# Kernel tuning notes

Measured on AMD Instinct MI355X. Metric: run time of the kernel, lower is better.

The kernel has to match this reference:

```python
import jax, jax.numpy as jnp
import numpy as np

DIM = 192
HEADS = 6
WS = (6, 12)          # (lat, lon) window
INPUT_SHAPE = (186, 360)
TOW = INPUT_SHAPE[0] // WS[0]   # 31 latitude window types
N_WIN = WS[0] * WS[1]           # 72 tokens per window


def _position_index():
    """Earth-specific relative-position index (static, numpy)."""
    ws0, ws1 = WS
    coords_hi = np.arange(ws0)
    coords_hj = -np.arange(ws0) * ws0
    coords_w = np.arange(ws1)
    c1 = np.stack(np.meshgrid(coords_hi, coords_w, indexing='ij'))  # (2, ws0, ws1)
    c2 = np.stack(np.meshgrid(coords_hj, coords_w, indexing='ij'))
    f1 = c1.reshape(2, -1)
    f2 = c2.reshape(2, -1)
    coords = f1[:, :, None] - f2[:, None, :]      # (2, N, N)
    coords = coords.transpose(1, 2, 0).copy()     # (N, N, 2)
    coords[:, :, 1] += ws1 - 1                    # shift lon diff to >= 0
    coords[:, :, 0] *= 2 * ws1 - 1                # row stride in bias table
    return jnp.asarray(coords.sum(-1).reshape(-1))  # (N*N,) int


def setup_inputs() -> dict:
    key = jax.random.key(0)
    ks = jax.random.split(key, 6)
    B = 2
    nW = INPUT_SHAPE[1] // WS[1]          # 30
    B_ = B * TOW * nW                     # 1860
    table_rows = (2 * WS[1] - 1) * WS[0] * WS[0]  # 828
    return {
        "x": jax.random.normal(ks[0], (B_, N_WIN, DIM), dtype=jnp.float32),
        "mask": jnp.zeros((nW, N_WIN, N_WIN), dtype=jnp.float32),
        "w_qkv": jax.random.normal(ks[1], (DIM, 3 * DIM), dtype=jnp.float32) * 0.02,
        "b_qkv": jnp.zeros((3 * DIM,), dtype=jnp.float32),
        "w_out": jax.random.normal(ks[2], (DIM, DIM), dtype=jnp.float32) * 0.02,
        "b_out": jnp.zeros((DIM,), dtype=jnp.float32),
        "bias_table": jax.random.normal(ks[3], (table_rows, TOW, HEADS), dtype=jnp.float32) * 0.02,
    }


def reference(x, mask, w_qkv, b_qkv, w_out, b_out, bias_table):
    B_, N, dim = x.shape
    hd = dim // HEADS
    scale = hd ** -0.5
    # fused QKV projection
    qkv = (x @ w_qkv + b_qkv).reshape(B_, N, 3, HEADS, hd)
    qkv = qkv.transpose(2, 0, 3, 1, 4)            # (3, B_, H, N, hd)
    q, k, v = qkv[0] * scale, qkv[1], qkv[2]
    attn = jnp.einsum('bhnd,bhmd->bhnm', q, k)    # (B_, H, N, N)
    # earth-specific bias: gather table rows by relative-position index,
    # tiled across the window batch exactly as the torch code's .repeat()
    rep = B_ // TOW
    pos = _position_index()                       # (N*N,)
    bias = bias_table[jnp.tile(pos, rep)]         # (rep*N*N, TOW, H)
    bias = bias.reshape(N, N, -1, HEADS).transpose(2, 3, 0, 1)  # (B_, H, N, N)
    attn = attn + bias
    # window mask (broadcast over groups of nW lon-windows)
    nW = mask.shape[0]
    attn = attn.reshape(B_ // nW, nW, HEADS, N, N) + mask[None, :, None]
    attn = attn.reshape(B_, HEADS, N, N)
    attn = jax.nn.softmax(attn, axis=-1)          # dropout is identity (p=0 / eval)
    out = jnp.einsum('bhnm,bhmd->bhnd', attn, v)  # (B_, H, N, hd)
    out = out.transpose(0, 2, 1, 3).reshape(B_, N, dim)
    return out @ w_out + b_out
```

## Files before the change

kernel.cpp:

```cpp
#include <hip/hip_runtime.h>
#include <cstddef>

typedef short bf16x8 __attribute__((ext_vector_type(8)));
typedef float f32x4  __attribute__((ext_vector_type(4)));

namespace {
constexpr float QSCALE = 0.17677669529663687f;

constexpr size_t BQKV_OFF = 0;
constexpr size_t WOUT_OFF = 576 * 384 * 2;
constexpr size_t BQG_OFF  = WOUT_OFF + 192 * 384 * 2;

constexpr int AXS   = 392;
constexpr int AX_H  = 0;
constexpr int Q2A_H = 72 * AXS;
constexpr int K2A_H = Q2A_H + 6 * 72 * 32;
constexpr int V2A_H = K2A_H + 6 * 72 * 40;
constexpr int HALF_TOT = V2A_H + 6 * 32 * 104;
constexpr int PB_H  = 828 * 6 * 2;
constexpr int LDSA_BYTES = HALF_TOT * 2;
}

__device__ __forceinline__ unsigned short f2bf(float f) {
  unsigned int u = __builtin_bit_cast(unsigned int, f);
  return (unsigned short)((u + 0x7FFFu + ((u >> 16) & 1u)) >> 16);
}
__device__ __forceinline__ float bf2f(unsigned short h) {
  unsigned int u = ((unsigned int)h) << 16;
  return __builtin_bit_cast(float, u);
}
__device__ __forceinline__ int moffv(int i) { return (i < 4) ? i * 16 : 56; }

__global__ __launch_bounds__(256)
void prep_kernel(const float* __restrict__ wqkv, const float* __restrict__ bqkv,
                 const float* __restrict__ wout, unsigned char* __restrict__ ws) {
  int t = blockIdx.x * 256 + threadIdx.x;
  unsigned short* Bq = (unsigned short*)(ws + BQKV_OFF);
  unsigned short* Bo = (unsigned short*)(ws + WOUT_OFF);
  float* bqg = (float*)(ws + BQG_OFF);
  if (t < 576 * 384) {
    int n = t / 384, kk = t % 384;
    int ksrc = kk % 192, part = kk / 192;
    int h = n / 96, r96 = n % 96, kind = r96 / 32, d = r96 % 32;
    float w = wqkv[(size_t)ksrc * 576 + kind * 192 + h * 32 + d];
    if (kind == 0) w *= QSCALE;
    unsigned short hi = f2bf(w);
    Bq[t] = part ? f2bf(w - bf2f(hi)) : hi;
  } else if (t < 576 * 384 + 192 * 384) {
    int t2 = t - 576 * 384;
    int n = t2 / 384, kk = t2 % 384, ksrc = kk % 192, part = kk / 192;
    float w = wout[(size_t)ksrc * 192 + n];
    unsigned short hi = f2bf(w);
    Bo[t2] = part ? f2bf(w - bf2f(hi)) : hi;
  } else if (t < 576 * 384 + 192 * 384 + 576) {
    int n = t - (576 * 384 + 192 * 384);
    int h = n / 96, r96 = n % 96, kind = r96 / 32, d = r96 % 32;
    float b = bqkv[kind * 192 + h * 32 + d];
    if (kind == 0) b *= QSCALE;
    bqg[n] = b;
  }
}

template<int NM>
__device__ __forceinline__ void qkv_wave(unsigned short* sm, const unsigned short* __restrict__ Bq,
                                         const float* __restrict__ bqg, int ntb3, int m0idx,
                                         int lanen, int quad) {
  #pragma unroll 1
  for (int p = 0; p < 3; ++p) {
    const int nbase = 192 * p;
    f32x4 acc[3][NM];
    #pragma unroll
    for (int nt = 0; nt < 3; ++nt)
      #pragma unroll
      for (int mi = 0; mi < NM; ++mi)
        acc[nt][mi] = (f32x4){0.f, 0.f, 0.f, 0.f};
    #pragma unroll 1
    for (int reg = 0; reg < 3; ++reg) {
      const int ab = (reg == 2) ? 192 : 0;
      const int bb = (reg == 1) ? 192 : 0;
      bf16x8 a[NM][6];
      #pragma unroll
      for (int mi = 0; mi < NM; ++mi) {
        const unsigned short* ap = sm + AX_H + (moffv(m0idx + mi) + lanen) * AXS + ab + quad * 8;
        #pragma unroll
        for (int s = 0; s < 6; ++s)
          a[mi][s] = *(const bf16x8*)(ap + 32 * s);
      }
      #pragma unroll
      for (int nt = 0; nt < 3; ++nt) {
        const unsigned short* bp = Bq + (size_t)(nbase + (ntb3 + nt) * 16 + lanen) * 384 + bb + quad * 8;
        #pragma unroll
        for (int s = 0; s < 6; ++s) {
          bf16x8 bfr = *(const bf16x8*)(bp + 32 * s);
          #pragma unroll
          for (int mi = 0; mi < NM; ++mi)
            acc[nt][mi] = __builtin_amdgcn_mfma_f32_16x16x32_bf16(a[mi][s], bfr, acc[nt][mi], 0, 0, 0);
        }
      }
    }
    #pragma unroll 1
    for (int nt = 0; nt < 3; ++nt) {
      const int ng = ntb3 + nt;
      const float bias = bqg[nbase + ng * 16 + lanen];
      const int hh = 2 * p + (ng >= 6 ? 1 : 0);
      const int w96 = (ng % 6) * 16;
      #pragma unroll
      for (int mi = 0; mi < NM; ++mi) {
        const int mo = moffv(m0idx + mi);
        if (w96 < 64) {
          unsigned short* dst;
          int stride, d;
          if (w96 < 32) { dst = sm + Q2A_H + hh * 2304; stride = 32; d = w96 + lanen; }
          else          { dst = sm + K2A_H + hh * 2880; stride = 40; d = w96 - 32 + lanen; }
          #pragma unroll
          for (int r = 0; r < 4; ++r)
            dst[(mo + quad * 4 + r) * stride + d] = f2bf(acc[nt][mi][r] + bias);
        } else {
          const int d = w96 - 64 + lanen;
          ushort4 hv;
          hv.x = f2bf(acc[nt][mi][0] + bias); hv.y = f2bf(acc[nt][mi][1] + bias);
          hv.z = f2bf(acc[nt][mi][2] + bias); hv.w = f2bf(acc[nt][mi][3] + bias);
          *(ushort4*)(sm + V2A_H + hh * 3328 + d * 104 + mo + quad * 4) = hv;
        }
      }
    }
  }
}

__global__ __launch_bounds__(512)
__attribute__((amdgpu_waves_per_eu(2, 2)))
void attn_kernel(const float* __restrict__ x, const float* __restrict__ mask,
                 const float* __restrict__ btab, const unsigned char* __restrict__ ws,
                 float* __restrict__ out) {
  extern __shared__ unsigned short sm[];
  const int w = blockIdx.x, tid = threadIdx.x;
  const int lane = tid & 63, ty = tid >> 6;
  const int lanen = lane & 15, quad = lane >> 4;
  const int mrow = w % 30, tlat = w % 31, w31 = w / 31;
  const float* xw = x + (size_t)w * (72 * 192);
  const float* maskw = mask + (size_t)mrow * (72 * 72);
  const unsigned short* Bq = (const unsigned short*)(ws + BQKV_OFF);
  const float* bqg = (const float*)(ws + BQG_OFF);

  for (int i = tid; i < 3456; i += 512) {
    int r = i / 48, c4 = i % 48;
    float4 v = *(const float4*)(xw + r * 192 + c4 * 4);
    unsigned short h0 = f2bf(v.x), h1 = f2bf(v.y), h2 = f2bf(v.z), h3 = f2bf(v.w);
    ushort4 hv; hv.x = h0; hv.y = h1; hv.z = h2; hv.w = h3;
    ushort4 lv;
    lv.x = f2bf(v.x - bf2f(h0)); lv.y = f2bf(v.y - bf2f(h1));
    lv.z = f2bf(v.z - bf2f(h2)); lv.w = f2bf(v.w - bf2f(h3));
    *(ushort4*)(sm + AX_H + r * AXS + c4 * 4) = hv;
    *(ushort4*)(sm + AX_H + r * AXS + 192 + c4 * 4) = lv;
  }
  for (int i = tid; i < 9984; i += 512)
    ((unsigned int*)(sm + V2A_H))[i] = 0u;
  __syncthreads();

  {
    const int mg = ty >> 2, ntb3 = (ty & 3) * 3;
    if (mg == 0) qkv_wave<3>(sm, Bq, bqg, ntb3, 0, lanen, quad);
    else         qkv_wave<2>(sm, Bq, bqg, ntb3, 3, lanen, quad);
  }
  __syncthreads();

  float* btabs = (float*)sm;
  for (int i = tid; i < 4968; i += 512)
    btabs[i] = btab[(size_t)(i / 6) * 186 + tlat * 6 + (i % 6)];
  for (int i = tid; i < 6656; i += 512)
    ((unsigned int*)(sm + PB_H))[i] = 0u;
  __syncthreads();

  unsigned short* pb = sm + PB_H + ty * 1664;
  #pragma unroll 1
  for (int j = ty; j < 30; j += 8) {
    const int hh = j / 5, mo = moffv(j % 5);
    const unsigned short* q2 = sm + Q2A_H + hh * 2304;
    const unsigned short* k2 = sm + K2A_H + hh * 2880;
    const unsigned short* v2 = sm + V2A_H + hh * 3328;

    bf16x8 afr = *(const bf16x8*)(q2 + (mo + lanen) * 32 + quad * 8);
    f32x4 s[5];
    #pragma unroll
    for (int t = 0; t < 5; ++t) {
      int no = (t < 4) ? t * 16 : 64;
      bf16x8 bfr = *(const bf16x8*)(k2 + (no + lanen) * 40 + quad * 8);
      s[t] = (f32x4){0.f, 0.f, 0.f, 0.f};
      s[t] = __builtin_amdgcn_mfma_f32_16x16x32_bf16(afr, bfr, s[t], 0, 0, 0);
    }
    float lg[5][4];
    #pragma unroll
    for (int t = 0; t < 5; ++t) {
      int ct = ((t < 4) ? t * 16 : 64) + lanen;
      #pragma unroll
      for (int r = 0; r < 4; ++r) {
        if (ct < 72) {
          int m = mo + quad * 4 + r;
          unsigned int e = (unsigned)(m % 6); e = e ? 6u - e : 0u;
          unsigned int T = 864u * e + 60u * (unsigned)ct + (unsigned)w31;
          if (T >= 5184u) T -= 5184u;
          unsigned int p1 = T / 72u, p2 = T - 72u * p1;
          unsigned int i1 = p1 / 12u, j1 = p1 - 12u * i1;
          unsigned int i2 = p2 / 12u, j2 = p2 - 12u * i2;
          int rowb = (int)((i1 + 6u * i2) * 23u + j1) - (int)j2 + 11;
          float bv = btabs[rowb * 6 + hh];
          lg[t][r] = s[t][r] + bv + maskw[m * 72 + ct];
        } else lg[t][r] = -1e30f;
      }
    }
    #pragma unroll
    for (int r = 0; r < 4; ++r) {
      float mx = fmaxf(fmaxf(fmaxf(lg[0][r], lg[1][r]), fmaxf(lg[2][r], lg[3][r])), lg[4][r]);
      #pragma unroll
      for (int o = 8; o > 0; o >>= 1) mx = fmaxf(mx, __shfl_xor(mx, o));
      float sum = 0.f;
      #pragma unroll
      for (int t = 0; t < 5; ++t) { lg[t][r] = __expf(lg[t][r] - mx); sum += lg[t][r]; }
      #pragma unroll
      for (int o = 8; o > 0; o >>= 1) sum += __shfl_xor(sum, o);
      float inv = 1.0f / sum;
      #pragma unroll
      for (int t = 0; t < 5; ++t) {
        int ct = ((t < 4) ? t * 16 : 64) + lanen;
        if (ct < 72) pb[(quad * 4 + r) * 104 + ct] = f2bf(lg[t][r] * inv);
      }
    }
    f32x4 o2[2];
    o2[0] = (f32x4){0.f, 0.f, 0.f, 0.f}; o2[1] = (f32x4){0.f, 0.f, 0.f, 0.f};
    #pragma unroll
    for (int ks = 0; ks < 3; ++ks) {
      bf16x8 pfr = *(const bf16x8*)(pb + lanen * 104 + ks * 32 + quad * 8);
      #pragma unroll
      for (int n2 = 0; n2 < 2; ++n2) {
        bf16x8 vfr = *(const bf16x8*)(v2 + (n2 * 16 + lanen) * 104 + ks * 32 + quad * 8);
        o2[n2] = __builtin_amdgcn_mfma_f32_16x16x32_bf16(pfr, vfr, o2[n2], 0, 0, 0);
      }
    }
    #pragma unroll
    for (int n2 = 0; n2 < 2; ++n2) {
      int col = hh * 32 + n2 * 16 + lanen;
      #pragma unroll
      for (int r = 0; r < 4; ++r)
        out[((size_t)w * 72 + mo + quad * 4 + r) * 192 + col] = o2[n2][r];
    }
  }
}

__global__ __launch_bounds__(256)
__attribute__((amdgpu_waves_per_eu(2, 2)))
void outproj_kernel(const unsigned char* __restrict__ ws, const float* __restrict__ bout,
                    float* __restrict__ out) {
  __shared__ unsigned short Ax[72 * AXS];
  const int w = blockIdx.x, tid = threadIdx.x;
  const int lane = tid & 63, ty = tid >> 6;
  const int lanen = lane & 15, quad = lane >> 4;
  const unsigned short* Bo = (const unsigned short*)(ws + WOUT_OFF);
  float* rows = out + (size_t)w * (72 * 192);

  for (int i = tid; i < 3456; i += 256) {
    int r = i / 48, c4 = i % 48;
    float4 v = *(const float4*)(rows + r * 192 + c4 * 4);
    unsigned short h0 = f2bf(v.x), h1 = f2bf(v.y), h2 = f2bf(v.z), h3 = f2bf(v.w);
    ushort4 hv; hv.x = h0; hv.y = h1; hv.z = h2; hv.w = h3;
    ushort4 lv;
    lv.x = f2bf(v.x - bf2f(h0)); lv.y = f2bf(v.y - bf2f(h1));
    lv.z = f2bf(v.z - bf2f(h2)); lv.w = f2bf(v.w - bf2f(h3));
    *(ushort4*)(Ax + r * AXS + c4 * 4) = hv;
    *(ushort4*)(Ax + r * AXS + 192 + c4 * 4) = lv;
  }
  __syncthreads();

  const int ntb3 = ty * 3;
  f32x4 acc[3][5];
  #pragma unroll
  for (int nt = 0; nt < 3; ++nt)
    #pragma unroll
    for (int mi = 0; mi < 5; ++mi)
      acc[nt][mi] = (f32x4){0.f, 0.f, 0.f, 0.f};

  #pragma unroll 1
  for (int reg = 0; reg < 3; ++reg) {
    const int ab = (reg == 2) ? 192 : 0;
    const int bb = (reg == 1) ? 192 : 0;
    #pragma unroll 1
    for (int hk = 0; hk < 2; ++hk) {
      bf16x8 a[5][3];
      #pragma unroll
      for (int mi = 0; mi < 5; ++mi) {
        const unsigned short* ap = Ax + (moffv(mi) + lanen) * AXS + ab + hk * 96 + quad * 8;
        #pragma unroll
        for (int s2 = 0; s2 < 3; ++s2)
          a[mi][s2] = *(const bf16x8*)(ap + 32 * s2);
      }
      #pragma unroll
      for (int nt = 0; nt < 3; ++nt) {
        const unsigned short* bp = Bo + (size_t)((ntb3 + nt) * 16 + lanen) * 384 + bb + hk * 96 + quad * 8;
        #pragma unroll
        for (int s2 = 0; s2 < 3; ++s2) {
          bf16x8 bfr = *(const bf16x8*)(bp + 32 * s2);
          #pragma unroll
          for (int mi = 0; mi < 5; ++mi)
            acc[nt][mi] = __builtin_amdgcn_mfma_f32_16x16x32_bf16(a[mi][s2], bfr, acc[nt][mi], 0, 0, 0);
        }
      }
    }
  }

  #pragma unroll 1
  for (int nt = 0; nt < 3; ++nt) {
    const float bias = bout[(ntb3 + nt) * 16 + lanen];
    #pragma unroll
    for (int mi = 0; mi < 5; ++mi) {
      const int mo = moffv(mi);
      #pragma unroll
      for (int r = 0; r < 4; ++r)
        rows[(mo + quad * 4 + r) * 192 + (ntb3 + nt) * 16 + lanen] = acc[nt][mi][r] + bias;
    }
  }
}

extern "C" void kernel_launch(void* const* d_in, const int* in_sizes, int n_in,
                              void* d_out, int out_size, void* d_ws, size_t ws_size,
                              hipStream_t stream) {
  const float* x    = (const float*)d_in[0];
  const float* mask = (const float*)d_in[1];
  const float* wqkv = (const float*)d_in[2];
  const float* bqkv = (const float*)d_in[3];
  const float* wout = (const float*)d_in[4];
  const float* bout = (const float*)d_in[5];
  const float* btab = (const float*)d_in[6];
  float* out = (float*)d_out;
  unsigned char* ws = (unsigned char*)d_ws;
  const int nwindows = in_sizes[0] / (72 * 192);

  prep_kernel<<<dim3(1155), dim3(256), 0, stream>>>(wqkv, bqkv, wout, ws);

  (void)hipFuncSetAttribute((const void*)attn_kernel,
                            hipFuncAttributeMaxDynamicSharedMemorySize, LDSA_BYTES);
  attn_kernel<<<dim3(nwindows), dim3(512), LDSA_BYTES, stream>>>(x, mask, btab, ws, out);

  outproj_kernel<<<dim3(nwindows), dim3(256), 0, stream>>>(ws, bout, out);
}
```

Baseline: 815.1 us.

## Split fused attention kernel into QKV, per-head attention, and output projection kernels

Splits the single per-window attention kernel, which held QKV, bias table and probabilities in a large dynamic LDS block, into three kernels. A QKV projection kernel writes bf16 Q/K/V per window and head to a global workspace. A per-(window, head) attention kernel with small LDS then computes scores, gathers the bias directly from global memory, applies softmax and multiplies by V. The output projection moves to 512 threads with the shared split-GEMM helper. The aim is lower LDS use per block and more parallel blocks, at the cost of extra global round-trips for Q/K/V and one more launch.

```diff
diff --git a/kernel.cpp b/kernel.cpp
--- a/kernel.cpp
+++ b/kernel.cpp
@@ -10,15 +10,11 @@
 constexpr size_t BQKV_OFF = 0;
 constexpr size_t WOUT_OFF = 576 * 384 * 2;
 constexpr size_t BQG_OFF  = WOUT_OFF + 192 * 384 * 2;
-
-constexpr int AXS   = 392;
-constexpr int AX_H  = 0;
-constexpr int Q2A_H = 72 * AXS;
-constexpr int K2A_H = Q2A_H + 6 * 72 * 32;
-constexpr int V2A_H = K2A_H + 6 * 72 * 40;
-constexpr int HALF_TOT = V2A_H + 6 * 32 * 104;
-constexpr int PB_H  = 828 * 6 * 2;
-constexpr int LDSA_BYTES = HALF_TOT * 2;
+constexpr size_t QG_OFF   = BQG_OFF + 576 * 4;
+constexpr size_t KG_OFF   = QG_OFF + (size_t)11160 * 2304 * 2;
+constexpr size_t VG_OFF   = KG_OFF + (size_t)11160 * 2304 * 2;
+
+constexpr int AXS = 392;
 }
 
 __device__ __forceinline__ unsigned short f2bf(float f) {
@@ -62,85 +58,73 @@
 }
 
 template<int NM>
-__device__ __forceinline__ void qkv_wave(unsigned short* sm, const unsigned short* __restrict__ Bq,
-                                         const float* __restrict__ bqg, int ntb3, int m0idx,
-                                         int lanen, int quad) {
+__device__ __forceinline__ void split_gemm(const unsigned short* __restrict__ sm,
+                                           const unsigned short* __restrict__ Bt,
+                                           int ngb, int m0idx, int lanen, int quad,
+                                           f32x4 (&acc)[3][NM]) {
+  #pragma unroll
+  for (int nt = 0; nt < 3; ++nt)
+    #pragma unroll
+    for (int mi = 0; mi < NM; ++mi)
+      acc[nt][mi] = (f32x4){0.f, 0.f, 0.f, 0.f};
   #pragma unroll 1
-  for (int p = 0; p < 3; ++p) {
-    const int nbase = 192 * p;
-    f32x4 acc[3][NM];
-    #pragma unroll
-    for (int nt = 0; nt < 3; ++nt)
+  for (int reg = 0; reg < 3; ++reg) {
+    const int ab = (reg == 2) ? 192 : 0;
+    const int bb = (reg == 1) ? 192 : 0;
+    #pragma unroll 2
+    for (int s = 0; s < 6; ++s) {
+      bf16x8 a[NM];
       #pragma unroll
       for (int mi = 0; mi < NM; ++mi)
-        acc[nt][mi] = (f32x4){0.f, 0.f, 0.f, 0.f};
-    #pragma unroll 1
-    for (int reg = 0; reg < 3; ++reg) {
-      const int ab = (reg == 2) ? 192 : 0;
-      const int bb = (reg == 1) ? 192 : 0;
-      bf16x8 a[NM][6];
-      #pragma unroll
-      for (int mi = 0; mi < NM; ++mi) {
-        const unsigned short* ap = sm + AX_H + (moffv(m0idx + mi) + lanen) * AXS + ab + quad * 8;
-        #pragma unroll
-        for (int s = 0; s < 6; ++s)
-          a[mi][s] = *(const bf16x8*)(ap + 32 * s);
-      }
+        a[mi] = *(const bf16x8*)(sm + (moffv(m0idx + mi) + lanen) * AXS + ab + 32 * s + quad * 8);
       #pragma unroll
       for (int nt = 0; nt < 3; ++nt) {
-        const unsigned short* bp = Bq + (size_t)(nbase + (ntb3 + nt) * 16 + lanen) * 384 + bb + quad * 8;
+        bf16x8 bfr = *(const bf16x8*)(Bt + (size_t)((ngb + nt) * 16 + lanen) * 384 + bb + 32 * s + quad * 8);
         #pragma unroll
-        for (int s = 0; s < 6; ++s) {
-          bf16x8 bfr = *(const bf16x8*)(bp + 32 * s);
-          #pragma unroll
-          for (int mi = 0; mi < NM; ++mi)
-            acc[nt][mi] = __builtin_amdgcn_mfma_f32_16x16x32_bf16(a[mi][s], bfr, acc[nt][mi], 0, 0, 0);
-        }
+        for (int mi = 0; mi < NM; ++mi)
+          acc[nt][mi] = __builtin_amdgcn_mfma_f32_16x16x32_bf16(a[mi], bfr, acc[nt][mi], 0, 0, 0);
       }
     }
-    #pragma unroll 1
-    for (int nt = 0; nt < 3; ++nt) {
-      const int ng = ntb3 + nt;
-      const float bias = bqg[nbase + ng * 16 + lanen];
-      const int hh = 2 * p + (ng >= 6 ? 1 : 0);
-      const int w96 = (ng % 6) * 16;
-      #pragma unroll
-      for (int mi = 0; mi < NM; ++mi) {
-        const int mo = moffv(m0idx + mi);
-        if (w96 < 64) {
-          unsigned short* dst;
-          int stride, d;
-          if (w96 < 32) { dst = sm + Q2A_H + hh * 2304; stride = 32; d = w96 + lanen; }
-          else          { dst = sm + K2A_H + hh * 2880; stride = 40; d = w96 - 32 + lanen; }
-          #pragma unroll
-          for (int r = 0; r < 4; ++r)
-            dst[(mo + quad * 4 + r) * stride + d] = f2bf(acc[nt][mi][r] + bias);
-        } else {
-          const int d = w96 - 64 + lanen;
-          ushort4 hv;
-          hv.x = f2bf(acc[nt][mi][0] + bias); hv.y = f2bf(acc[nt][mi][1] + bias);
-          hv.z = f2bf(acc[nt][mi][2] + bias); hv.w = f2bf(acc[nt][mi][3] + bias);
-          *(ushort4*)(sm + V2A_H + hh * 3328 + d * 104 + mo + quad * 4) = hv;
-        }
+  }
+}
+
+template<int NM>
+__device__ __forceinline__ void qkv_epi(const f32x4 (&acc)[3][NM], const float* __restrict__ bqg,
+                                        unsigned short* __restrict__ qg, unsigned short* __restrict__ kg,
+                                        unsigned short* __restrict__ vg,
+                                        int w, int ngb, int m0idx, int lanen, int quad) {
+  #pragma unroll 1
+  for (int nt = 0; nt < 3; ++nt) {
+    const int ng = ngb + nt;
+    const int h = ng / 6, w6 = (ng % 6) * 16;
+    const float bias = bqg[ng * 16 + lanen];
+    const size_t base = (size_t)(w * 6 + h) * 2304;
+    #pragma unroll
+    for (int mi = 0; mi < NM; ++mi) {
+      const int mo = moffv(m0idx + mi);
+      if (w6 < 64) {
+        unsigned short* dst = ((w6 < 32) ? qg : kg) + base + (w6 & 31) + lanen;
+        #pragma unroll
+        for (int r = 0; r < 4; ++r)
+          dst[(size_t)(mo + quad * 4 + r) * 32] = f2bf(acc[nt][mi][r] + bias);
+      } else {
+        const int d = (w6 - 64) + lanen;
+        ushort4 hv;
+        hv.x = f2bf(acc[nt][mi][0] + bias); hv.y = f2bf(acc[nt][mi][1] + bias);
+        hv.z = f2bf(acc[nt][mi][2] + bias); hv.w = f2bf(acc[nt][mi][3] + bias);
+        *(ushort4*)(vg + base + (size_t)d * 72 + mo + quad * 4) = hv;
       }
     }
   }
 }
 
 __global__ __launch_bounds__(512)
-__attribute__((amdgpu_waves_per_eu(2, 2)))
-void attn_kernel(const float* __restrict__ x, const float* __restrict__ mask,
-                 const float* __restrict__ btab, const unsigned char* __restrict__ ws,
-                 float* __restrict__ out) {
-  extern __shared__ unsigned short sm[];
+void qkv_kernel(const float* __restrict__ x, unsigned char* __restrict__ ws) {
+  __shared__ unsigned short sm[72 * AXS];
   const int w = blockIdx.x, tid = threadIdx.x;
   const int lane = tid & 63, ty = tid >> 6;
   const int lanen = lane & 15, quad = lane >> 4;
-  const int mrow = w % 30, tlat = w % 31, w31 = w / 31;
   const float* xw = x + (size_t)w * (72 * 192);
-  const float* maskw = mask + (size_t)mrow * (72 * 72);
-  const unsigned short* Bq = (const unsigned short*)(ws + BQKV_OFF);
-  const float* bqg = (const float*)(ws + BQG_OFF);
 
   for (int i = tid; i < 3456; i += 512) {
     int r = i / 48, c4 = i % 48;
@@ -150,104 +134,128 @@
     ushort4 lv;
     lv.x = f2bf(v.x - bf2f(h0)); lv.y = f2bf(v.y - bf2f(h1));
     lv.z = f2bf(v.z - bf2f(h2)); lv.w = f2bf(v.w - bf2f(h3));
-    *(ushort4*)(sm + AX_H + r * AXS + c4 * 4) = hv;
-    *(ushort4*)(sm + AX_H + r * AXS + 192 + c4 * 4) = lv;
-  }
-  for (int i = tid; i < 9984; i += 512)
-    ((unsigned int*)(sm + V2A_H))[i] = 0u;
+    *(ushort4*)(sm + r * AXS + c4 * 4) = hv;
+    *(ushort4*)(sm + r * AXS + 192 + c4 * 4) = lv;
+  }
   __syncthreads();
 
+  const unsigned short* Bq = (const unsigned short*)(ws + BQKV_OFF);
+  const float* bqg = (const float*)(ws + BQG_OFF);
+  unsigned short* qg = (unsigned short*)(ws + QG_OFF);
+  unsigned short* kg = (unsigned short*)(ws + KG_OFF);
+  unsigned short* vg = (unsigned short*)(ws + VG_OFF);
+
+  const int mg = ty >> 2, nq = ty & 3;
+  #pragma unroll 1
+  for (int it = 0; it < 3; ++it) {
+    const int ngb = (nq + 4 * it) * 3;
+    if (mg == 0) {
+      f32x4 acc[3][3];
+      split_gemm<3>(sm, Bq, ngb, 0, lanen, quad, acc);
+      qkv_epi<3>(acc, bqg, qg, kg, vg, w, ngb, 0, lanen, quad);
+    } else {
+      f32x4 acc[3][2];
+      split_gemm<2>(sm, Bq, ngb, 3, lanen, quad, acc);
+      qkv_epi<2>(acc, bqg, qg, kg, vg, w, ngb, 3, lanen, quad);
+    }
+  }
+}
+
+__global__ __launch_bounds__(320)
+void attn_core(const float* __restrict__ mask, const float* __restrict__ btab,
+               const unsigned char* __restrict__ ws, float* __restrict__ out) {
+  __shared__ unsigned short V2[32 * 104];
+  __shared__ unsigned short PB[5 * 16 * 104];
+  const int b = blockIdx.x, w = b / 6, hh = b - w * 6;
+  const int tid = threadIdx.x, lane = tid & 63, ty = tid >> 6;
+  const int lanen = lane & 15, quad = lane >> 4;
+  const int mrow = w % 30, tlat = w % 31, w31 = w / 31;
+  const unsigned short* qg = (const unsigned short*)(ws + QG_OFF) + (size_t)b * 2304;
+  const unsigned short* kg = (const unsigned short*)(ws + KG_OFF) + (size_t)b * 2304;
+  const unsigned short* vg = (const unsigned short*)(ws + VG_OFF) + (size_t)b * 2304;
+  const float* maskw = mask + (size_t)mrow * 5184;
+
+  for (int i = tid; i < 416; i += 320) {
+    int r = i / 13, c = i - r * 13;
+    uint4 z = make_uint4(0u, 0u, 0u, 0u);
+    *(uint4*)(V2 + r * 104 + c * 8) = (c < 9) ? *(const uint4*)(vg + r * 72 + c * 8) : z;
+  }
   {
-    const int mg = ty >> 2, ntb3 = (ty & 3) * 3;
-    if (mg == 0) qkv_wave<3>(sm, Bq, bqg, ntb3, 0, lanen, quad);
-    else         qkv_wave<2>(sm, Bq, bqg, ntb3, 3, lanen, quad);
+    int wv = tid >> 6, rr = (tid >> 2) & 15, c = tid & 3;
+    *(uint4*)(PB + wv * 1664 + rr * 104 + 72 + c * 8) = make_uint4(0u, 0u, 0u, 0u);
   }
   __syncthreads();
 
-  float* btabs = (float*)sm;
-  for (int i = tid; i < 4968; i += 512)
-    btabs[i] = btab[(size_t)(i / 6) * 186 + tlat * 6 + (i % 6)];
-  for (int i = tid; i < 6656; i += 512)
-    ((unsigned int*)(sm + PB_H))[i] = 0u;
-  __syncthreads();
-
-  unsigned short* pb = sm + PB_H + ty * 1664;
-  #pragma unroll 1
-  for (int j = ty; j < 30; j += 8) {
-    const int hh = j / 5, mo = moffv(j % 5);
-    const unsigned short* q2 = sm + Q2A_H + hh * 2304;
-    const unsigned short* k2 = sm + K2A_H + hh * 2880;
-    const unsigned short* v2 = sm + V2A_H + hh * 3328;
-
-    bf16x8 afr = *(const bf16x8*)(q2 + (mo + lanen) * 32 + quad * 8);
-    f32x4 s[5];
-    #pragma unroll
-    for (int t = 0; t < 5; ++t) {
-      int no = (t < 4) ? t * 16 : 64;
-      bf16x8 bfr = *(const bf16x8*)(k2 + (no + lanen) * 40 + quad * 8);
-      s[t] = (f32x4){0.f, 0.f, 0.f, 0.f};
-      s[t] = __builtin_amdgcn_mfma_f32_16x16x32_bf16(afr, bfr, s[t], 0, 0, 0);
-    }
-    float lg[5][4];
+  const int mo = moffv(ty);
+  unsigned short* pb = PB + ty * 1664;
+
+  bf16x8 afr = *(const bf16x8*)(qg + (mo + lanen) * 32 + quad * 8);
+  f32x4 s[5];
+  #pragma unroll
+  for (int t = 0; t < 5; ++t) {
+    int no = (t < 4) ? t * 16 : 64;
+    bf16x8 bfr = *(const bf16x8*)(kg + (no + lanen) * 32 + quad * 8);
+    s[t] = (f32x4){0.f, 0.f, 0.f, 0.f};
+    s[t] = __builtin_amdgcn_mfma_f32_16x16x32_bf16(afr, bfr, s[t], 0, 0, 0);
+  }
+  float lg[5][4];
+  #pragma unroll
+  for (int t = 0; t < 5; ++t) {
+    int ct = ((t < 4) ? t * 16 : 64) + lanen;
+    #pragma unroll
+    for (int r = 0; r < 4; ++r) {
+      if (ct < 72) {
+        int m = mo + quad * 4 + r;
+        unsigned int e = (unsigned)(m % 6); e = e ? 6u - e : 0u;
+        unsigned int T = 864u * e + 60u * (unsigned)ct + (unsigned)w31;
+        if (T >= 5184u) T -= 5184u;
+        unsigned int p1 = T / 72u, p2 = T - 72u * p1;
+        unsigned int i1 = p1 / 12u, j1 = p1 - 12u * i1;
+        unsigned int i2 = p2 / 12u, j2 = p2 - 12u * i2;
+        int rowb = (int)((i1 + 6u * i2) * 23u + j1) - (int)j2 + 11;
+        float bv = btab[(size_t)rowb * 186 + tlat * 6 + hh];
+        lg[t][r] = s[t][r] + bv + maskw[m * 72 + ct];
+      } else lg[t][r] = -1e30f;
+    }
+  }
+  #pragma unroll
+  for (int r = 0; r < 4; ++r) {
+    float mx = fmaxf(fmaxf(fmaxf(lg[0][r], lg[1][r]), fmaxf(lg[2][r], lg[3][r])), lg[4][r]);
+    #pragma unroll
+    for (int o = 8; o > 0; o >>= 1) mx = fmaxf(mx, __shfl_xor(mx, o));
+    float sum = 0.f;
+    #pragma unroll
+    for (int t = 0; t < 5; ++t) { lg[t][r] = __expf(lg[t][r] - mx); sum += lg[t][r]; }
+    #pragma unroll
+    for (int o = 8; o > 0; o >>= 1) sum += __shfl_xor(sum, o);
+    float inv = 1.0f / sum;
     #pragma unroll
     for (int t = 0; t < 5; ++t) {
       int ct = ((t < 4) ? t * 16 : 64) + lanen;
-      #pragma unroll
-      for (int r = 0; r < 4; ++r) {
-        if (ct < 72) {
-          int m = mo + quad * 4 + r;
-          unsigned int e = (unsigned)(m % 6); e = e ? 6u - e : 0u;
-          unsigned int T = 864u * e + 60u * (unsigned)ct + (unsigned)w31;
-          if (T >= 5184u) T -= 5184u;
-          unsigned int p1 = T / 72u, p2 = T - 72u * p1;
-          unsigned int i1 = p1 / 12u, j1 = p1 - 12u * i1;
-          unsigned int i2 = p2 / 12u, j2 = p2 - 12u * i2;
-          int rowb = (int)((i1 + 6u * i2) * 23u + j1) - (int)j2 + 11;
-          float bv = btabs[rowb * 6 + hh];
-          lg[t][r] = s[t][r] + bv + maskw[m * 72 + ct];
-        } else lg[t][r] = -1e30f;
-      }
-    }
-    #pragma unroll
-    for (int r = 0; r < 4; ++r) {
-      float mx = fmaxf(fmaxf(fmaxf(lg[0][r], lg[1][r]), fmaxf(lg[2][r], lg[3][r])), lg[4][r]);
-      #pragma unroll
-      for (int o = 8; o > 0; o >>= 1) mx = fmaxf(mx, __shfl_xor(mx, o));
-      float sum = 0.f;
-      #pragma unroll
-      for (int t = 0; t < 5; ++t) { lg[t][r] = __expf(lg[t][r] - mx); sum += lg[t][r]; }
-      #pragma unroll
-      for (int o = 8; o > 0; o >>= 1) sum += __shfl_xor(sum, o);
-      float inv = 1.0f / sum;
-      #pragma unroll
-      for (int t = 0; t < 5; ++t) {
-        int ct = ((t < 4) ? t * 16 : 64) + lanen;
-        if (ct < 72) pb[(quad * 4 + r) * 104 + ct] = f2bf(lg[t][r] * inv);
-      }
-    }
-    f32x4 o2[2];
-    o2[0] = (f32x4){0.f, 0.f, 0.f, 0.f}; o2[1] = (f32x4){0.f, 0.f, 0.f, 0.f};
-    #pragma unroll
-    for (int ks = 0; ks < 3; ++ks) {
-      bf16x8 pfr = *(const bf16x8*)(pb + lanen * 104 + ks * 32 + quad * 8);
-      #pragma unroll
-      for (int n2 = 0; n2 < 2; ++n2) {
-        bf16x8 vfr = *(const bf16x8*)(v2 + (n2 * 16 + lanen) * 104 + ks * 32 + quad * 8);
-        o2[n2] = __builtin_amdgcn_mfma_f32_16x16x32_bf16(pfr, vfr, o2[n2], 0, 0, 0);
-      }
-    }
+      if (ct < 72) pb[(quad * 4 + r) * 104 + ct] = f2bf(lg[t][r] * inv);
+    }
+  }
+  f32x4 o2[2];
+  o2[0] = (f32x4){0.f, 0.f, 0.f, 0.f}; o2[1] = (f32x4){0.f, 0.f, 0.f, 0.f};
+  #pragma unroll
+  for (int ks = 0; ks < 3; ++ks) {
+    bf16x8 pfr = *(const bf16x8*)(pb + lanen * 104 + ks * 32 + quad * 8);
     #pragma unroll
     for (int n2 = 0; n2 < 2; ++n2) {
-      int col = hh * 32 + n2 * 16 + lanen;
-      #pragma unroll
-      for (int r = 0; r < 4; ++r)
-        out[((size_t)w * 72 + mo + quad * 4 + r) * 192 + col] = o2[n2][r];
-    }
-  }
-}
-
-__global__ __launch_bounds__(256)
-__attribute__((amdgpu_waves_per_eu(2, 2)))
+      bf16x8 vfr = *(const bf16x8*)(V2 + (n2 * 16 + lanen) * 104 + ks * 32 + quad * 8);
+      o2[n2] = __builtin_amdgcn_mfma_f32_16x16x32_bf16(pfr, vfr, o2[n2], 0, 0, 0);
+    }
+  }
+  #pragma unroll
+  for (int n2 = 0; n2 < 2; ++n2) {
+    int col = hh * 32 + n2 * 16 + lanen;
+    #pragma unroll
+    for (int r = 0; r < 4; ++r)
+      out[((size_t)w * 72 + mo + quad * 4 + r) * 192 + col] = o2[n2][r];
+  }
+}
+
+__global__ __launch_bounds__(512)
 void outproj_kernel(const unsigned char* __restrict__ ws, const float* __restrict__ bout,
                     float* __restrict__ out) {
   __shared__ unsigned short Ax[72 * AXS];
@@ -257,7 +265,7 @@
   const unsigned short* Bo = (const unsigned short*)(ws + WOUT_OFF);
   float* rows = out + (size_t)w * (72 * 192);
 
-  for (int i = tid; i < 3456; i += 256) {
+  for (int i = tid; i < 3456; i += 512) {
     int r = i / 48, c4 = i % 48;
     float4 v = *(const float4*)(rows + r * 192 + c4 * 4);
     unsigned short h0 = f2bf(v.x), h1 = f2bf(v.y), h2 = f2bf(v.z), h3 = f2bf(v.w);
@@ -270,51 +278,37 @@
   }
   __syncthreads();
 
-  const int ntb3 = ty * 3;
-  f32x4 acc[3][5];
-  #pragma unroll
-  for (int nt = 0; nt < 3; ++nt)
-    #pragma unroll
-    for (int mi = 0; mi < 5; ++mi)
-      acc[nt][mi] = (f32x4){0.f, 0.f, 0.f, 0.f};
-
-  #pragma unroll 1
-  for (int reg = 0; reg < 3; ++reg) {
-    const int ab = (reg == 2) ? 192 : 0;
-    const int bb = (reg == 1) ? 192 : 0;
+  const int mg = ty >> 2, nq = ty & 3;
+  const int ngb = nq * 3;
+  if (mg == 0) {
+    f32x4 acc[3][3];
+    split_gemm<3>(Ax, Bo, ngb, 0, lanen, quad, acc);
     #pragma unroll 1
-    for (int hk = 0; hk < 2; ++hk) {
-      bf16x8 a[5][3];
+    for (int nt = 0; nt < 3; ++nt) {
+      const int n16 = (ngb + nt) * 16;
+      const float bias = bout[n16 + lanen];
       #pragma unroll
-      for (int mi = 0; mi < 5; ++mi) {
-        const unsigned short* ap = Ax + (moffv(mi) + lanen) * AXS + ab + hk * 96 + quad * 8;
+      for (int mi = 0; mi < 3; ++mi) {
+        const int mo = moffv(mi);
         #pragma unroll
-        for (int s2 = 0; s2 < 3; ++s2)
-          a[mi][s2] = *(const bf16x8*)(ap + 32 * s2);
+        for (int r = 0; r < 4; ++r)
+          rows[(size_t)(mo + quad * 4 + r) * 192 + n16 + lanen] = acc[nt][mi][r] + bias;
       }
+    }
+  } else {
+    f32x4 acc[3][2];
+    split_gemm<2>(Ax, Bo, ngb, 3, lanen, quad, acc);
+    #pragma unroll 1
+    for (int nt = 0; nt < 3; ++nt) {
+      const int n16 = (ngb + nt) * 16;
+      const float bias = bout[n16 + lanen];
       #pragma unroll
-      for (int nt = 0; nt < 3; ++nt) {
-        const unsigned short* bp = Bo + (size_t)((ntb3 + nt) * 16 + lanen) * 384 + bb + hk * 96 + quad * 8;
+      for (int mi = 0; mi < 2; ++mi) {
+        const int mo = moffv(3 + mi);
         #pragma unroll
-        for (int s2 = 0; s2 < 3; ++s2) {
-          bf16x8 bfr = *(const bf16x8*)(bp + 32 * s2);
-          #pragma unroll
-          for (int mi = 0; mi < 5; ++mi)
-            acc[nt][mi] = __builtin_amdgcn_mfma_f32_16x16x32_bf16(a[mi][s2], bfr, acc[nt][mi], 0, 0, 0);
-        }
+        for (int r = 0; r < 4; ++r)
+          rows[(size_t)(mo + quad * 4 + r) * 192 + n16 + lanen] = acc[nt][mi][r] + bias;
       }
-    }
-  }
-
-  #pragma unroll 1
-  for (int nt = 0; nt < 3; ++nt) {
-    const float bias = bout[(ntb3 + nt) * 16 + lanen];
-    #pragma unroll
-    for (int mi = 0; mi < 5; ++mi) {
-      const int mo = moffv(mi);
-      #pragma unroll
-      for (int r = 0; r < 4; ++r)
-        rows[(mo + quad * 4 + r) * 192 + (ntb3 + nt) * 16 + lanen] = acc[nt][mi][r] + bias;
     }
   }
 }
@@ -334,10 +328,7 @@
   const int nwindows = in_sizes[0] / (72 * 192);
 
   prep_kernel<<<dim3(1155), dim3(256), 0, stream>>>(wqkv, bqkv, wout, ws);
-
-  (void)hipFuncSetAttribute((const void*)attn_kernel,
-                            hipFuncAttributeMaxDynamicSharedMemorySize, LDSA_BYTES);
-  attn_kernel<<<dim3(nwindows), dim3(512), LDSA_BYTES, stream>>>(x, mask, btab, ws, out);
-
-  outproj_kernel<<<dim3(nwindows), dim3(256), 0, stream>>>(ws, bout, out);
-}
+  qkv_kernel<<<dim3(nwindows), dim3(512), 0, stream>>>(x, ws);
+  attn_core<<<dim3(nwindows * 6), dim3(320), 0, stream>>>(mask, btab, ws, out);
+  outproj_kernel<<<dim3(nwindows), dim3(512), 0, stream>>>(ws, bout, out);
+}
```

After: 864.7 us. 1.06x slower.
